# Kernel optimization log

Measured on AMD Instinct MI355X. Metric: run time of the kernel, lower is better.

## Reference

```python
import jax, jax.numpy as jnp
import numpy as np

EPS = 1e-5

def bn(x, g, b, mu, var):
    # inference-mode BatchNorm2d (InPlaceABNSync, activation='none')
    scale = g * jax.lax.rsqrt(var + EPS)
    shift = b - mu * scale
    return x * scale[None, :, None, None] + shift[None, :, None, None]

def conv1x1(x, w):
    # w: [C_out, C_in]; x: [B, C_in, H, W]
    return jnp.einsum('oc,bchw->bohw', w, x)

def block(x, w1, g1, b1, m1, v1, w2, g2, b2, m2, v2):
    # conv1x1 -> BN -> ReLU -> conv1x1 -> BN -> ReLU
    h = jax.nn.relu(bn(conv1x1(x, w1), g1, b1, m1, v1))
    return jax.nn.relu(bn(conv1x1(h, w2), g2, b2, m2, v2))

def setup_inputs() -> dict:
    key = jax.random.key(0)
    ks = jax.random.split(key, 24)
    B, HID, H, W = 8, 10, 512, 512
    MID = 32
    d = {}
    d['xf']  = jax.random.normal(ks[0], (B, HID, H, W), jnp.float32)
    d['xh1'] = jax.random.normal(ks[1], (B, HID, H, W), jnp.float32)
    d['xh2'] = jax.random.normal(ks[2], (B, HID, H, W), jnp.float32)
    def mk_bn(k, c):
        k1, k2, k3, k4 = jax.random.split(k, 4)
        return (jax.random.normal(k1, (c,), jnp.float32) * 0.1 + 1.0,
                jax.random.normal(k2, (c,), jnp.float32) * 0.1,
                jax.random.normal(k3, (c,), jnp.float32) * 0.1,
                jnp.abs(jax.random.normal(k4, (c,), jnp.float32)) * 0.5 + 0.5)
    # conv_hf params
    d['w_hf1'] = jax.random.normal(ks[3], (MID, 2 * HID), jnp.float32) * (1.0 / np.sqrt(2 * HID))
    d['g_hf1'], d['b_hf1'], d['m_hf1'], d['v_hf1'] = mk_bn(ks[4], MID)
    d['w_hf2'] = jax.random.normal(ks[5], (HID, MID), jnp.float32) * (1.0 / np.sqrt(MID))
    d['g_hf2'], d['b_hf2'], d['m_hf2'], d['v_hf2'] = mk_bn(ks[6], HID)
    # conv_update params
    d['w_up1'] = jax.random.normal(ks[7], (MID, 2 * HID), jnp.float32) * (1.0 / np.sqrt(2 * HID))
    d['g_up1'], d['b_up1'], d['m_up1'], d['v_up1'] = mk_bn(ks[8], MID)
    d['w_up2'] = jax.random.normal(ks[9], (HID, MID), jnp.float32) * (1.0 / np.sqrt(MID))
    d['g_up2'], d['b_up2'], d['m_up2'], d['v_up2'] = mk_bn(ks[10], HID)
    return d

def reference(xf, xh1, xh2,
              w_hf1, g_hf1, b_hf1, m_hf1, v_hf1,
              w_hf2, g_hf2, b_hf2, m_hf2, v_hf2,
              w_up1, g_up1, b_up1, m_up1, v_up1,
              w_up2, g_up2, b_up2, m_up2, v_up2):
    message = block(jnp.concatenate([xh1, xh2], axis=1),
                    w_hf1, g_hf1, b_hf1, m_hf1, v_hf1,
                    w_hf2, g_hf2, b_hf2, m_hf2, v_hf2)
    xf_new = block(jnp.concatenate([xf, message], axis=1),
                   w_up1, g_up1, b_up1, m_up1, v_up1,
                   w_up2, g_up2, b_up2, m_up2, v_up2)
    return (xf_new, message)
```

## Files before the change

### kernel.cpp

```cpp
#include <hip/hip_runtime.h>

#define EPS_BN 1e-5f
#define HW2 131072u
#define MSG_OFF 10485760u

typedef unsigned int u32;
typedef __fp16 h2 __attribute__((ext_vector_type(2)));

union W32 { u32 u; float f; h2 h; };

__device__ __forceinline__ float asf(u32 u){ W32 w; w.u = u; return w.f; }
__device__ __forceinline__ h2    ash(u32 u){ W32 w; w.u = u; return w.h; }
__device__ __forceinline__ u32 packh(float a, float b){
  W32 w; w.h.x = (__fp16)a; w.h.y = (__fp16)b; return w.u;
}

#if __has_builtin(__builtin_amdgcn_fdot2)
__device__ __forceinline__ float dot2(h2 a, h2 b, float c){
  return __builtin_amdgcn_fdot2(a, b, c, false);
}
#else
__device__ __forceinline__ float dot2(h2 a, h2 b, float c){
  return c + (float)a.x * (float)b.x + (float)a.y * (float)b.y;
}
#endif

#if __has_builtin(__builtin_amdgcn_cvt_pkrtz)
__device__ __forceinline__ h2 pk(float a, float b){ return __builtin_amdgcn_cvt_pkrtz(a, b); }
#else
__device__ __forceinline__ h2 pk(float a, float b){ h2 r; r.x = (__fp16)a; r.y = (__fp16)b; return r; }
#endif


extern "C" __global__ void prep_kernel(
  const float* __restrict__ w1, const float* __restrict__ g1, const float* __restrict__ b1, const float* __restrict__ m1, const float* __restrict__ v1,
  const float* __restrict__ w2, const float* __restrict__ g2, const float* __restrict__ b2, const float* __restrict__ m2, const float* __restrict__ v2,
  const float* __restrict__ w3, const float* __restrict__ g3, const float* __restrict__ b3, const float* __restrict__ m3, const float* __restrict__ v3,
  const float* __restrict__ w4, const float* __restrict__ g4, const float* __restrict__ b4, const float* __restrict__ m4, const float* __restrict__ v4,
  u32* __restrict__ ws)
{
  const int t = threadIdx.x;
  for (int i = t; i < 320; i += 256){ int cp = i >> 5, o = i & 31;
    float sc = g1[o] * rsqrtf(v1[o] + EPS_BN);
    ws[i] = packh(w1[o*20 + 2*cp] * sc, w1[o*20 + 2*cp + 1] * sc); }
  for (int i = t; i < 32; i += 256){
    float sc = g1[i] * rsqrtf(v1[i] + EPS_BN);
    W32 w; w.f = b1[i] - m1[i] * sc; ws[320 + i] = w.u; }
  for (int i = t; i < 256; i += 256){ int cp = i >> 4, o = i & 15; u32 val = 0u;
    if (o < 10){ float sc = g2[o] * rsqrtf(v2[o] + EPS_BN);
      val = packh(w2[o*32 + 2*cp] * sc, w2[o*32 + 2*cp + 1] * sc); }
    ws[352 + i] = val; }
  for (int i = t; i < 16; i += 256){ W32 w; w.f = 0.f;
    if (i < 10){ float sc = g2[i] * rsqrtf(v2[i] + EPS_BN); w.f = b2[i] - m2[i] * sc; }
    ws[608 + i] = w.u; }
  for (int i = t; i < 320; i += 256){ int cp = i >> 5, o = i & 31;
    float sc = g3[o] * rsqrtf(v3[o] + EPS_BN);
    ws[624 + i] = packh(w3[o*20 + 2*cp] * sc, w3[o*20 + 2*cp + 1] * sc); }
  for (int i = t; i < 32; i += 256){
    float sc = g3[i] * rsqrtf(v3[i] + EPS_BN);
    W32 w; w.f = b3[i] - m3[i] * sc; ws[944 + i] = w.u; }
  for (int i = t; i < 256; i += 256){ int cp = i >> 4, o = i & 15; u32 val = 0u;
    if (o < 10){ float sc = g4[o] * rsqrtf(v4[o] + EPS_BN);
      val = packh(w4[o*32 + 2*cp] * sc, w4[o*32 + 2*cp + 1] * sc); }
    ws[976 + i] = val; }
  for (int i = t; i < 16; i += 256){ W32 w; w.f = 0.f;
    if (i < 10){ float sc = g4[i] * rsqrtf(v4[i] + EPS_BN); w.f = b4[i] - m4[i] * sc; }
    ws[1232 + i] = w.u; }
}

#define DO4(AX, AY, HX, HY, Q, O0) \
  { h2 w0_ = ash((Q).x), w1_ = ash((Q).y), w2_ = ash((Q).z), w3_ = ash((Q).w); \
    AX[(O0)+0] = dot2(HX, w0_, AX[(O0)+0]); AY[(O0)+0] = dot2(HY, w0_, AY[(O0)+0]); \
    AX[(O0)+1] = dot2(HX, w1_, AX[(O0)+1]); AY[(O0)+1] = dot2(HY, w1_, AY[(O0)+1]); \
    AX[(O0)+2] = dot2(HX, w2_, AX[(O0)+2]); AY[(O0)+2] = dot2(HY, w2_, AY[(O0)+2]); \
    AX[(O0)+3] = dot2(HX, w3_, AX[(O0)+3]); AY[(O0)+3] = dot2(HY, w3_, AY[(O0)+3]); }

extern "C" __global__ __launch_bounds__(256) void fused_kernel(
  const float2* __restrict__ xf, const float2* __restrict__ xh1, const float2* __restrict__ xh2,
  const u32* __restrict__ wsp, float2* __restrict__ out)
{
  __shared__ __align__(16) u32 s[1248];
  for (int i = threadIdx.x; i < 1248; i += 256) s[i] = wsp[i];
  __syncthreads();

  const unsigned p  = blockIdx.x * 256u + threadIdx.x;
  const unsigned b  = p >> 17;
  const unsigned hw = p & (HW2 - 1u);
  const size_t base = (size_t)b * (10u * HW2) + hw;
  const float2* A1 = xh1 + base;
  const float2* A2 = xh2 + base;
  const float2* AF = xf  + base;

  float ax[32], ay[32];
  h2 px[10], py[10];

  #pragma unroll
  for (int o = 0; o < 32; o++){ float t = asf(s[320 + o]); ax[o] = t; ay[o] = t; }
  #pragma unroll
  for (int cp = 0; cp < 5; cp++){
    float2 c0 = A1[(size_t)(2*cp) * HW2];
    float2 c1 = A1[(size_t)(2*cp + 1) * HW2];
    px[cp] = pk(c0.x, c1.x); py[cp] = pk(c0.y, c1.y);
  }
  #pragma unroll
  for (int cp = 0; cp < 5; cp++){
    float2 c0 = A2[(size_t)(2*cp) * HW2];
    float2 c1 = A2[(size_t)(2*cp + 1) * HW2];
    px[5+cp] = pk(c0.x, c1.x); py[5+cp] = pk(c0.y, c1.y);
  }
  #pragma unroll
  for (int cp = 0; cp < 10; cp++){
    const uint4* wr = (const uint4*)&s[cp * 32];
    h2 hx = px[cp], hy = py[cp];
    #pragma unroll
    for (int j = 0; j < 8; j++){ uint4 q = wr[j]; DO4(ax, ay, hx, hy, q, 4*j); }
  }
  #pragma unroll
  for (int o = 0; o < 32; o++){ ax[o] = fmaxf(ax[o], 0.f); ay[o] = fmaxf(ay[o], 0.f); }

  float mx[10], my[10];
  #pragma unroll
  for (int o = 0; o < 10; o++){ float t = asf(s[608 + o]); mx[o] = t; my[o] = t; }
  h2 qx[16], qy[16];
  #pragma unroll
  for (int k = 0; k < 16; k++){ qx[k] = pk(ax[2*k], ax[2*k+1]); qy[k] = pk(ay[2*k], ay[2*k+1]); }
  #pragma unroll
  for (int cp = 0; cp < 16; cp++){
    const uint4* wr = (const uint4*)&s[352 + cp * 16];
    h2 hx = qx[cp], hy = qy[cp];
    uint4 q0 = wr[0]; DO4(mx, my, hx, hy, q0, 0);
    uint4 q1 = wr[1]; DO4(mx, my, hx, hy, q1, 4);
    uint4 q2 = wr[2];
    { h2 w0_ = ash(q2.x), w1_ = ash(q2.y);
      mx[8] = dot2(hx, w0_, mx[8]); my[8] = dot2(hy, w0_, my[8]);
      mx[9] = dot2(hx, w1_, mx[9]); my[9] = dot2(hy, w1_, my[9]); }
  }
  #pragma unroll
  for (int o = 0; o < 10; o++){ mx[o] = fmaxf(mx[o], 0.f); my[o] = fmaxf(my[o], 0.f); }
  #pragma unroll
  for (int o = 0; o < 10; o++){
    float2 r; r.x = mx[o]; r.y = my[o];
    out[MSG_OFF + base + (size_t)o * HW2] = r;
  }

  #pragma unroll
  for (int o = 0; o < 32; o++){ float t = asf(s[944 + o]); ax[o] = t; ay[o] = t; }
  #pragma unroll
  for (int cp = 0; cp < 5; cp++){
    float2 c0 = AF[(size_t)(2*cp) * HW2];
    float2 c1 = AF[(size_t)(2*cp + 1) * HW2];
    px[cp] = pk(c0.x, c1.x); py[cp] = pk(c0.y, c1.y);
  }
  #pragma unroll
  for (int k = 0; k < 5; k++){
    px[5+k] = pk(mx[2*k], mx[2*k+1]); py[5+k] = pk(my[2*k], my[2*k+1]);
  }
  #pragma unroll
  for (int cp = 0; cp < 10; cp++){
    const uint4* wr = (const uint4*)&s[624 + cp * 32];
    h2 hx = px[cp], hy = py[cp];
    #pragma unroll
    for (int j = 0; j < 8; j++){ uint4 q = wr[j]; DO4(ax, ay, hx, hy, q, 4*j); }
  }
  #pragma unroll
  for (int o = 0; o < 32; o++){ ax[o] = fmaxf(ax[o], 0.f); ay[o] = fmaxf(ay[o], 0.f); }

  float ox[10], oy[10];
  #pragma unroll
  for (int o = 0; o < 10; o++){ float t = asf(s[1232 + o]); ox[o] = t; oy[o] = t; }
  #pragma unroll
  for (int k = 0; k < 16; k++){ qx[k] = pk(ax[2*k], ax[2*k+1]); qy[k] = pk(ay[2*k], ay[2*k+1]); }
  #pragma unroll
  for (int cp = 0; cp < 16; cp++){
    const uint4* wr = (const uint4*)&s[976 + cp * 16];
    h2 hx = qx[cp], hy = qy[cp];
    uint4 q0 = wr[0]; DO4(ox, oy, hx, hy, q0, 0);
    uint4 q1 = wr[1]; DO4(ox, oy, hx, hy, q1, 4);
    uint4 q2 = wr[2];
    { h2 w0_ = ash(q2.x), w1_ = ash(q2.y);
      ox[8] = dot2(hx, w0_, ox[8]); oy[8] = dot2(hy, w0_, oy[8]);
      ox[9] = dot2(hx, w1_, ox[9]); oy[9] = dot2(hy, w1_, oy[9]); }
  }
  #pragma unroll
  for (int o = 0; o < 10; o++){
    float2 r; r.x = fmaxf(ox[o], 0.f); r.y = fmaxf(oy[o], 0.f);
    out[base + (size_t)o * HW2] = r;
  }
}

extern "C" void kernel_launch(void* const* d_in, const int* in_sizes, int n_in,
                              void* d_out, int out_size, void* d_ws, size_t ws_size,
                              hipStream_t stream)
{
  u32* ws = (u32*)d_ws;
  prep_kernel<<<1, 256, 0, stream>>>(
    (const float*)d_in[3],  (const float*)d_in[4],  (const float*)d_in[5],  (const float*)d_in[6],  (const float*)d_in[7],
    (const float*)d_in[8],  (const float*)d_in[9],  (const float*)d_in[10], (const float*)d_in[11], (const float*)d_in[12],
    (const float*)d_in[13], (const float*)d_in[14], (const float*)d_in[15], (const float*)d_in[16], (const float*)d_in[17],
    (const float*)d_in[18], (const float*)d_in[19], (const float*)d_in[20], (const float*)d_in[21], (const float*)d_in[22],
    ws);

  fused_kernel<<<4096, 256, 0, stream>>>(
    (const float2*)d_in[0], (const float2*)d_in[1], (const float2*)d_in[2],
    ws, (float2*)d_out);
}
```

Before: 381.5 us.

## Process four pixels per thread with float4 loads to amortize LDS weight reads

Each thread now handles four consecutive pixels instead of two, using float4 global loads and stores and halving the grid. Every weight fetched from shared memory is reused across four pixels, which cuts LDS traffic per FLOP, and bias initialization is folded into the first dot product. The xf load is moved earlier to overlap with compute, and launch bounds request two blocks per CU. The cost is much higher register pressure (a 32x4 accumulator array plus 16x4 packed halves), which may cause spills or lower occupancy on this memory-bound kernel.

```diff
diff --git a/kernel.cpp b/kernel.cpp
--- a/kernel.cpp
+++ b/kernel.cpp
@@ -1,8 +1,8 @@
 #include <hip/hip_runtime.h>
 
 #define EPS_BN 1e-5f
-#define HW2 131072u
-#define MSG_OFF 10485760u
+#define HW4 65536u
+#define MSG_OFF4 5242880u
 
 typedef unsigned int u32;
 typedef __fp16 h2 __attribute__((ext_vector_type(2)));
@@ -68,123 +68,166 @@
     ws[1232 + i] = w.u; }
 }
 
-#define DO4(AX, AY, HX, HY, Q, O0) \
+#define DO4x(A, H, Q, O0) \
   { h2 w0_ = ash((Q).x), w1_ = ash((Q).y), w2_ = ash((Q).z), w3_ = ash((Q).w); \
-    AX[(O0)+0] = dot2(HX, w0_, AX[(O0)+0]); AY[(O0)+0] = dot2(HY, w0_, AY[(O0)+0]); \
-    AX[(O0)+1] = dot2(HX, w1_, AX[(O0)+1]); AY[(O0)+1] = dot2(HY, w1_, AY[(O0)+1]); \
-    AX[(O0)+2] = dot2(HX, w2_, AX[(O0)+2]); AY[(O0)+2] = dot2(HY, w2_, AY[(O0)+2]); \
-    AX[(O0)+3] = dot2(HX, w3_, AX[(O0)+3]); AY[(O0)+3] = dot2(HY, w3_, AY[(O0)+3]); }
-
-extern "C" __global__ __launch_bounds__(256) void fused_kernel(
-  const float2* __restrict__ xf, const float2* __restrict__ xh1, const float2* __restrict__ xh2,
-  const u32* __restrict__ wsp, float2* __restrict__ out)
+    _Pragma("unroll") for (int j_ = 0; j_ < 4; j_++){ \
+      A[(O0)+0][j_] = dot2(H[j_], w0_, A[(O0)+0][j_]); \
+      A[(O0)+1][j_] = dot2(H[j_], w1_, A[(O0)+1][j_]); \
+      A[(O0)+2][j_] = dot2(H[j_], w2_, A[(O0)+2][j_]); \
+      A[(O0)+3][j_] = dot2(H[j_], w3_, A[(O0)+3][j_]); } }
+
+#define DO4i(A, H, Q, O0, BB) \
+  { h2 w0_ = ash((Q).x), w1_ = ash((Q).y), w2_ = ash((Q).z), w3_ = ash((Q).w); \
+    float b0_ = asf(s[(BB)+(O0)+0]), b1_ = asf(s[(BB)+(O0)+1]); \
+    float b2_ = asf(s[(BB)+(O0)+2]), b3_ = asf(s[(BB)+(O0)+3]); \
+    _Pragma("unroll") for (int j_ = 0; j_ < 4; j_++){ \
+      A[(O0)+0][j_] = dot2(H[j_], w0_, b0_); \
+      A[(O0)+1][j_] = dot2(H[j_], w1_, b1_); \
+      A[(O0)+2][j_] = dot2(H[j_], w2_, b2_); \
+      A[(O0)+3][j_] = dot2(H[j_], w3_, b3_); } }
+
+#define DO2x(A, H, Q2) \
+  { h2 w0_ = ash((Q2).x), w1_ = ash((Q2).y); \
+    _Pragma("unroll") for (int j_ = 0; j_ < 4; j_++){ \
+      A[8][j_] = dot2(H[j_], w0_, A[8][j_]); \
+      A[9][j_] = dot2(H[j_], w1_, A[9][j_]); } }
+
+#define DO2i(A, H, Q2, BB) \
+  { h2 w0_ = ash((Q2).x), w1_ = ash((Q2).y); \
+    float b8_ = asf(s[(BB)+8]), b9_ = asf(s[(BB)+9]); \
+    _Pragma("unroll") for (int j_ = 0; j_ < 4; j_++){ \
+      A[8][j_] = dot2(H[j_], w0_, b8_); \
+      A[9][j_] = dot2(H[j_], w1_, b9_); } }
+
+extern "C" __global__ __launch_bounds__(256, 2) void fused_kernel(
+  const float4* __restrict__ xf, const float4* __restrict__ xh1, const float4* __restrict__ xh2,
+  const u32* __restrict__ wsp, float4* __restrict__ out)
 {
   __shared__ __align__(16) u32 s[1248];
   for (int i = threadIdx.x; i < 1248; i += 256) s[i] = wsp[i];
   __syncthreads();
 
   const unsigned p  = blockIdx.x * 256u + threadIdx.x;
-  const unsigned b  = p >> 17;
-  const unsigned hw = p & (HW2 - 1u);
-  const size_t base = (size_t)b * (10u * HW2) + hw;
-  const float2* A1 = xh1 + base;
-  const float2* A2 = xh2 + base;
-  const float2* AF = xf  + base;
-
-  float ax[32], ay[32];
-  h2 px[10], py[10];
-
-  #pragma unroll
-  for (int o = 0; o < 32; o++){ float t = asf(s[320 + o]); ax[o] = t; ay[o] = t; }
+  const unsigned b  = p >> 16;
+  const unsigned hw = p & (HW4 - 1u);
+  const size_t base = (size_t)b * (10u * HW4) + hw;
+  const float4* A1 = xh1 + base;
+  const float4* A2 = xh2 + base;
+  const float4* AF = xf  + base;
+
+  float a[32][4];
+  h2 ph[10][4];
+
   #pragma unroll
   for (int cp = 0; cp < 5; cp++){
-    float2 c0 = A1[(size_t)(2*cp) * HW2];
-    float2 c1 = A1[(size_t)(2*cp + 1) * HW2];
-    px[cp] = pk(c0.x, c1.x); py[cp] = pk(c0.y, c1.y);
+    float4 c0 = A1[(size_t)(2*cp)     * HW4];
+    float4 c1 = A1[(size_t)(2*cp + 1) * HW4];
+    ph[cp][0] = pk(c0.x, c1.x); ph[cp][1] = pk(c0.y, c1.y);
+    ph[cp][2] = pk(c0.z, c1.z); ph[cp][3] = pk(c0.w, c1.w);
   }
   #pragma unroll
   for (int cp = 0; cp < 5; cp++){
-    float2 c0 = A2[(size_t)(2*cp) * HW2];
-    float2 c1 = A2[(size_t)(2*cp + 1) * HW2];
-    px[5+cp] = pk(c0.x, c1.x); py[5+cp] = pk(c0.y, c1.y);
-  }
-  #pragma unroll
-  for (int cp = 0; cp < 10; cp++){
+    float4 c0 = A2[(size_t)(2*cp)     * HW4];
+    float4 c1 = A2[(size_t)(2*cp + 1) * HW4];
+    ph[5+cp][0] = pk(c0.x, c1.x); ph[5+cp][1] = pk(c0.y, c1.y);
+    ph[5+cp][2] = pk(c0.z, c1.z); ph[5+cp][3] = pk(c0.w, c1.w);
+  }
+
+  { const uint4* wr = (const uint4*)&s[0];
+    #pragma unroll
+    for (int jw = 0; jw < 8; jw++){ uint4 q = wr[jw]; DO4i(a, ph[0], q, 4*jw, 320); } }
+  #pragma unroll
+  for (int cp = 1; cp < 10; cp++){
     const uint4* wr = (const uint4*)&s[cp * 32];
-    h2 hx = px[cp], hy = py[cp];
-    #pragma unroll
-    for (int j = 0; j < 8; j++){ uint4 q = wr[j]; DO4(ax, ay, hx, hy, q, 4*j); }
-  }
-  #pragma unroll
-  for (int o = 0; o < 32; o++){ ax[o] = fmaxf(ax[o], 0.f); ay[o] = fmaxf(ay[o], 0.f); }
-
-  float mx[10], my[10];
-  #pragma unroll
-  for (int o = 0; o < 10; o++){ float t = asf(s[608 + o]); mx[o] = t; my[o] = t; }
-  h2 qx[16], qy[16];
-  #pragma unroll
-  for (int k = 0; k < 16; k++){ qx[k] = pk(ax[2*k], ax[2*k+1]); qy[k] = pk(ay[2*k], ay[2*k+1]); }
-  #pragma unroll
-  for (int cp = 0; cp < 16; cp++){
+    #pragma unroll
+    for (int jw = 0; jw < 8; jw++){ uint4 q = wr[jw]; DO4x(a, ph[cp], q, 4*jw); }
+  }
+  #pragma unroll
+  for (int o = 0; o < 32; o++){
+    #pragma unroll
+    for (int j = 0; j < 4; j++) a[o][j] = fmaxf(a[o][j], 0.f);
+  }
+
+  #pragma unroll
+  for (int cp = 0; cp < 5; cp++){
+    float4 c0 = AF[(size_t)(2*cp)     * HW4];
+    float4 c1 = AF[(size_t)(2*cp + 1) * HW4];
+    ph[cp][0] = pk(c0.x, c1.x); ph[cp][1] = pk(c0.y, c1.y);
+    ph[cp][2] = pk(c0.z, c1.z); ph[cp][3] = pk(c0.w, c1.w);
+  }
+
+  h2 qh[16][4];
+  #pragma unroll
+  for (int k = 0; k < 16; k++){
+    #pragma unroll
+    for (int j = 0; j < 4; j++) qh[k][j] = pk(a[2*k][j], a[2*k+1][j]);
+  }
+  float m[10][4];
+  { const uint4* wr = (const uint4*)&s[352];
+    uint4 q0 = wr[0]; DO4i(m, qh[0], q0, 0, 608);
+    uint4 q1 = wr[1]; DO4i(m, qh[0], q1, 4, 608);
+    uint4 q2 = wr[2]; DO2i(m, qh[0], q2, 608); }
+  #pragma unroll
+  for (int cp = 1; cp < 16; cp++){
     const uint4* wr = (const uint4*)&s[352 + cp * 16];
-    h2 hx = qx[cp], hy = qy[cp];
-    uint4 q0 = wr[0]; DO4(mx, my, hx, hy, q0, 0);
-    uint4 q1 = wr[1]; DO4(mx, my, hx, hy, q1, 4);
-    uint4 q2 = wr[2];
-    { h2 w0_ = ash(q2.x), w1_ = ash(q2.y);
-      mx[8] = dot2(hx, w0_, mx[8]); my[8] = dot2(hy, w0_, my[8]);
-      mx[9] = dot2(hx, w1_, mx[9]); my[9] = dot2(hy, w1_, my[9]); }
-  }
-  #pragma unroll
-  for (int o = 0; o < 10; o++){ mx[o] = fmaxf(mx[o], 0.f); my[o] = fmaxf(my[o], 0.f); }
+    uint4 q0 = wr[0]; DO4x(m, qh[cp], q0, 0);
+    uint4 q1 = wr[1]; DO4x(m, qh[cp], q1, 4);
+    uint4 q2 = wr[2]; DO2x(m, qh[cp], q2);
+  }
   #pragma unroll
   for (int o = 0; o < 10; o++){
-    float2 r; r.x = mx[o]; r.y = my[o];
-    out[MSG_OFF + base + (size_t)o * HW2] = r;
-  }
-
-  #pragma unroll
-  for (int o = 0; o < 32; o++){ float t = asf(s[944 + o]); ax[o] = t; ay[o] = t; }
-  #pragma unroll
-  for (int cp = 0; cp < 5; cp++){
-    float2 c0 = AF[(size_t)(2*cp) * HW2];
-    float2 c1 = AF[(size_t)(2*cp + 1) * HW2];
-    px[cp] = pk(c0.x, c1.x); py[cp] = pk(c0.y, c1.y);
-  }
+    #pragma unroll
+    for (int j = 0; j < 4; j++) m[o][j] = fmaxf(m[o][j], 0.f);
+  }
+  #pragma unroll
+  for (int o = 0; o < 10; o++){
+    float4 r; r.x = m[o][0]; r.y = m[o][1]; r.z = m[o][2]; r.w = m[o][3];
+    out[MSG_OFF4 + base + (size_t)o * HW4] = r;
+  }
+
   #pragma unroll
   for (int k = 0; k < 5; k++){
-    px[5+k] = pk(mx[2*k], mx[2*k+1]); py[5+k] = pk(my[2*k], my[2*k+1]);
-  }
-  #pragma unroll
-  for (int cp = 0; cp < 10; cp++){
+    #pragma unroll
+    for (int j = 0; j < 4; j++) ph[5+k][j] = pk(m[2*k][j], m[2*k+1][j]);
+  }
+  { const uint4* wr = (const uint4*)&s[624];
+    #pragma unroll
+    for (int jw = 0; jw < 8; jw++){ uint4 q = wr[jw]; DO4i(a, ph[0], q, 4*jw, 944); } }
+  #pragma unroll
+  for (int cp = 1; cp < 10; cp++){
     const uint4* wr = (const uint4*)&s[624 + cp * 32];
-    h2 hx = px[cp], hy = py[cp];
-    #pragma unroll
-    for (int j = 0; j < 8; j++){ uint4 q = wr[j]; DO4(ax, ay, hx, hy, q, 4*j); }
-  }
-  #pragma unroll
-  for (int o = 0; o < 32; o++){ ax[o] = fmaxf(ax[o], 0.f); ay[o] = fmaxf(ay[o], 0.f); }
-
-  float ox[10], oy[10];
-  #pragma unroll
-  for (int o = 0; o < 10; o++){ float t = asf(s[1232 + o]); ox[o] = t; oy[o] = t; }
-  #pragma unroll
-  for (int k = 0; k < 16; k++){ qx[k] = pk(ax[2*k], ax[2*k+1]); qy[k] = pk(ay[2*k], ay[2*k+1]); }
-  #pragma unroll
-  for (int cp = 0; cp < 16; cp++){
+    #pragma unroll
+    for (int jw = 0; jw < 8; jw++){ uint4 q = wr[jw]; DO4x(a, ph[cp], q, 4*jw); }
+  }
+  #pragma unroll
+  for (int o = 0; o < 32; o++){
+    #pragma unroll
+    for (int j = 0; j < 4; j++) a[o][j] = fmaxf(a[o][j], 0.f);
+  }
+
+  #pragma unroll
+  for (int k = 0; k < 16; k++){
+    #pragma unroll
+    for (int j = 0; j < 4; j++) qh[k][j] = pk(a[2*k][j], a[2*k+1][j]);
+  }
+  float oo[10][4];
+  { const uint4* wr = (const uint4*)&s[976];
+    uint4 q0 = wr[0]; DO4i(oo, qh[0], q0, 0, 1232);
+    uint4 q1 = wr[1]; DO4i(oo, qh[0], q1, 4, 1232);
+    uint4 q2 = wr[2]; DO2i(oo, qh[0], q2, 1232); }
+  #pragma unroll
+  for (int cp = 1; cp < 16; cp++){
     const uint4* wr = (const uint4*)&s[976 + cp * 16];
-    h2 hx = qx[cp], hy = qy[cp];
-    uint4 q0 = wr[0]; DO4(ox, oy, hx, hy, q0, 0);
-    uint4 q1 = wr[1]; DO4(ox, oy, hx, hy, q1, 4);
-    uint4 q2 = wr[2];
-    { h2 w0_ = ash(q2.x), w1_ = ash(q2.y);
-      ox[8] = dot2(hx, w0_, ox[8]); oy[8] = dot2(hy, w0_, oy[8]);
-      ox[9] = dot2(hx, w1_, ox[9]); oy[9] = dot2(hy, w1_, oy[9]); }
+    uint4 q0 = wr[0]; DO4x(oo, qh[cp], q0, 0);
+    uint4 q1 = wr[1]; DO4x(oo, qh[cp], q1, 4);
+    uint4 q2 = wr[2]; DO2x(oo, qh[cp], q2);
   }
   #pragma unroll
   for (int o = 0; o < 10; o++){
-    float2 r; r.x = fmaxf(ox[o], 0.f); r.y = fmaxf(oy[o], 0.f);
-    out[base + (size_t)o * HW2] = r;
+    float4 r;
+    r.x = fmaxf(oo[o][0], 0.f); r.y = fmaxf(oo[o][1], 0.f);
+    r.z = fmaxf(oo[o][2], 0.f); r.w = fmaxf(oo[o][3], 0.f);
+    out[base + (size_t)o * HW4] = r;
   }
 }
 
@@ -200,7 +243,7 @@
     (const float*)d_in[18], (const float*)d_in[19], (const float*)d_in[20], (const float*)d_in[21], (const float*)d_in[22],
     ws);
 
-  fused_kernel<<<4096, 256, 0, stream>>>(
-    (const float2*)d_in[0], (const float2*)d_in[1], (const float2*)d_in[2],
-    ws, (float2*)d_out);
-}
+  fused_kernel<<<2048, 256, 0, stream>>>(
+    (const float4*)d_in[0], (const float4*)d_in[1], (const float4*)d_in[2],
+    ws, (float4*)d_out);
+}
```

Result: slower. 390.0 us (+2.2%).

## Read folded weights directly from global memory, fold bias into first dot, hoist xf loads

Applied to the files above, without the earlier changes.

Removes the shared-memory staging of the 1248-word weight table and its block barrier. Weights are now read straight from the global workspace; they are uniform across the wavefront, so the compiler may turn them into scalar loads. Bias initialisation is folded into the first dot2 of each layer instead of a separate copy loop. The xf input loads are moved earlier, ahead of the message layer, to overlap their latency with compute. The cost is many more global/scalar loads per thread and higher register pressure from the earlier xf loads.

```diff
diff --git a/kernel.cpp b/kernel.cpp
--- a/kernel.cpp
+++ b/kernel.cpp
@@ -75,13 +75,20 @@
     AX[(O0)+2] = dot2(HX, w2_, AX[(O0)+2]); AY[(O0)+2] = dot2(HY, w2_, AY[(O0)+2]); \
     AX[(O0)+3] = dot2(HX, w3_, AX[(O0)+3]); AY[(O0)+3] = dot2(HY, w3_, AY[(O0)+3]); }
 
+#define DO4i(AX, AY, HX, HY, Q, O0, BB) \
+  { h2 w0_ = ash((Q).x), w1_ = ash((Q).y), w2_ = ash((Q).z), w3_ = ash((Q).w); \
+    float b0_ = asf(s[(BB)+(O0)+0]), b1_ = asf(s[(BB)+(O0)+1]); \
+    float b2_ = asf(s[(BB)+(O0)+2]), b3_ = asf(s[(BB)+(O0)+3]); \
+    AX[(O0)+0] = dot2(HX, w0_, b0_); AY[(O0)+0] = dot2(HY, w0_, b0_); \
+    AX[(O0)+1] = dot2(HX, w1_, b1_); AY[(O0)+1] = dot2(HY, w1_, b1_); \
+    AX[(O0)+2] = dot2(HX, w2_, b2_); AY[(O0)+2] = dot2(HY, w2_, b2_); \
+    AX[(O0)+3] = dot2(HX, w3_, b3_); AY[(O0)+3] = dot2(HY, w3_, b3_); }
+
 extern "C" __global__ __launch_bounds__(256) void fused_kernel(
   const float2* __restrict__ xf, const float2* __restrict__ xh1, const float2* __restrict__ xh2,
   const u32* __restrict__ wsp, float2* __restrict__ out)
 {
-  __shared__ __align__(16) u32 s[1248];
-  for (int i = threadIdx.x; i < 1248; i += 256) s[i] = wsp[i];
-  __syncthreads();
+  const u32* __restrict__ s = wsp;
 
   const unsigned p  = blockIdx.x * 256u + threadIdx.x;
   const unsigned b  = p >> 17;
@@ -95,8 +102,6 @@
   h2 px[10], py[10];
 
   #pragma unroll
-  for (int o = 0; o < 32; o++){ float t = asf(s[320 + o]); ax[o] = t; ay[o] = t; }
-  #pragma unroll
   for (int cp = 0; cp < 5; cp++){
     float2 c0 = A1[(size_t)(2*cp) * HW2];
     float2 c1 = A1[(size_t)(2*cp + 1) * HW2];
@@ -108,8 +113,13 @@
     float2 c1 = A2[(size_t)(2*cp + 1) * HW2];
     px[5+cp] = pk(c0.x, c1.x); py[5+cp] = pk(c0.y, c1.y);
   }
-  #pragma unroll
-  for (int cp = 0; cp < 10; cp++){
+
+  { const uint4* wr = (const uint4*)&s[0];
+    h2 hx = px[0], hy = py[0];
+    #pragma unroll
+    for (int j = 0; j < 8; j++){ uint4 q = wr[j]; DO4i(ax, ay, hx, hy, q, 4*j, 320); } }
+  #pragma unroll
+  for (int cp = 1; cp < 10; cp++){
     const uint4* wr = (const uint4*)&s[cp * 32];
     h2 hx = px[cp], hy = py[cp];
     #pragma unroll
@@ -118,14 +128,28 @@
   #pragma unroll
   for (int o = 0; o < 32; o++){ ax[o] = fmaxf(ax[o], 0.f); ay[o] = fmaxf(ay[o], 0.f); }
 
+  #pragma unroll
+  for (int cp = 0; cp < 5; cp++){
+    float2 c0 = AF[(size_t)(2*cp) * HW2];
+    float2 c1 = AF[(size_t)(2*cp + 1) * HW2];
+    px[cp] = pk(c0.x, c1.x); py[cp] = pk(c0.y, c1.y);
+  }
+
   float mx[10], my[10];
-  #pragma unroll
-  for (int o = 0; o < 10; o++){ float t = asf(s[608 + o]); mx[o] = t; my[o] = t; }
   h2 qx[16], qy[16];
   #pragma unroll
   for (int k = 0; k < 16; k++){ qx[k] = pk(ax[2*k], ax[2*k+1]); qy[k] = pk(ay[2*k], ay[2*k+1]); }
-  #pragma unroll
-  for (int cp = 0; cp < 16; cp++){
+  { const uint4* wr = (const uint4*)&s[352];
+    h2 hx = qx[0], hy = qy[0];
+    uint4 q0 = wr[0]; DO4i(mx, my, hx, hy, q0, 0, 608);
+    uint4 q1 = wr[1]; DO4i(mx, my, hx, hy, q1, 4, 608);
+    uint4 q2 = wr[2];
+    { h2 w0_ = ash(q2.x), w1_ = ash(q2.y);
+      float b8_ = asf(s[608+8]), b9_ = asf(s[608+9]);
+      mx[8] = dot2(hx, w0_, b8_); my[8] = dot2(hy, w0_, b8_);
+      mx[9] = dot2(hx, w1_, b9_); my[9] = dot2(hy, w1_, b9_); } }
+  #pragma unroll
+  for (int cp = 1; cp < 16; cp++){
     const uint4* wr = (const uint4*)&s[352 + cp * 16];
     h2 hx = qx[cp], hy = qy[cp];
     uint4 q0 = wr[0]; DO4(mx, my, hx, hy, q0, 0);
@@ -144,19 +168,15 @@
   }
 
   #pragma unroll
-  for (int o = 0; o < 32; o++){ float t = asf(s[944 + o]); ax[o] = t; ay[o] = t; }
-  #pragma unroll
-  for (int cp = 0; cp < 5; cp++){
-    float2 c0 = AF[(size_t)(2*cp) * HW2];
-    float2 c1 = AF[(size_t)(2*cp + 1) * HW2];
-    px[cp] = pk(c0.x, c1.x); py[cp] = pk(c0.y, c1.y);
-  }
-  #pragma unroll
   for (int k = 0; k < 5; k++){
     px[5+k] = pk(mx[2*k], mx[2*k+1]); py[5+k] = pk(my[2*k], my[2*k+1]);
   }
-  #pragma unroll
-  for (int cp = 0; cp < 10; cp++){
+  { const uint4* wr = (const uint4*)&s[624];
+    h2 hx = px[0], hy = py[0];
+    #pragma unroll
+    for (int j = 0; j < 8; j++){ uint4 q = wr[j]; DO4i(ax, ay, hx, hy, q, 4*j, 944); } }
+  #pragma unroll
+  for (int cp = 1; cp < 10; cp++){
     const uint4* wr = (const uint4*)&s[624 + cp * 32];
     h2 hx = px[cp], hy = py[cp];
     #pragma unroll
@@ -167,11 +187,18 @@
 
   float ox[10], oy[10];
   #pragma unroll
-  for (int o = 0; o < 10; o++){ float t = asf(s[1232 + o]); ox[o] = t; oy[o] = t; }
-  #pragma unroll
   for (int k = 0; k < 16; k++){ qx[k] = pk(ax[2*k], ax[2*k+1]); qy[k] = pk(ay[2*k], ay[2*k+1]); }
-  #pragma unroll
-  for (int cp = 0; cp < 16; cp++){
+  { const uint4* wr = (const uint4*)&s[976];
+    h2 hx = qx[0], hy = qy[0];
+    uint4 q0 = wr[0]; DO4i(ox, oy, hx, hy, q0, 0, 1232);
+    uint4 q1 = wr[1]; DO4i(ox, oy, hx, hy, q1, 4, 1232);
+    uint4 q2 = wr[2];
+    { h2 w0_ = ash(q2.x), w1_ = ash(q2.y);
+      float b8_ = asf(s[1232+8]), b9_ = asf(s[1232+9]);
+      ox[8] = dot2(hx, w0_, b8_); oy[8] = dot2(hy, w0_, b8_);
+      ox[9] = dot2(hx, w1_, b9_); oy[9] = dot2(hy, w1_, b9_); } }
+  #pragma unroll
+  for (int cp = 1; cp < 16; cp++){
     const uint4* wr = (const uint4*)&s[976 + cp * 16];
     h2 hx = qx[cp], hy = qy[cp];
     uint4 q0 = wr[0]; DO4(ox, oy, hx, hy, q0, 0);
```

New measurement: 393.1 us. 1.03x slower.

## Compute fused 1x1 conv blocks with MFMA 16x16x32 f16 instead of dot2

Applied to the files above, without the earlier changes.

Replaces the per-thread fdot2 accumulation of all four 1x1 convolutions with MFMA 16x16x32 f16 instructions. Each wave now processes 16-pixel tiles in a loop, and the prep kernel packs weights into MFMA operand layouts with permuted K ordering. Weights live in registers rather than shared memory. The aim is to remove the ALU bottleneck, in exchange for narrower 64-byte coalesced global accesses and a complex lane/channel mapping.

```diff
diff --git a/kernel.cpp b/kernel.cpp
--- a/kernel.cpp
+++ b/kernel.cpp
@@ -1,36 +1,34 @@
 #include <hip/hip_runtime.h>
 
 #define EPS_BN 1e-5f
-#define HW2 131072u
-#define MSG_OFF 10485760u
+#define PLANE  262144u
+#define IMG10  2621440u
+#define MSGF   20971520u
 
 typedef unsigned int u32;
 typedef __fp16 h2 __attribute__((ext_vector_type(2)));
+typedef _Float16 v8h __attribute__((ext_vector_type(8)));
+typedef float v4f __attribute__((ext_vector_type(4)));
 
 union W32 { u32 u; float f; h2 h; };
-
-__device__ __forceinline__ float asf(u32 u){ W32 w; w.u = u; return w.f; }
-__device__ __forceinline__ h2    ash(u32 u){ W32 w; w.u = u; return w.h; }
+union AB  { u32 u[4]; uint4 q; v8h h; };
+
 __device__ __forceinline__ u32 packh(float a, float b){
   W32 w; w.h.x = (__fp16)a; w.h.y = (__fp16)b; return w.u;
 }
 
-#if __has_builtin(__builtin_amdgcn_fdot2)
-__device__ __forceinline__ float dot2(h2 a, h2 b, float c){
-  return __builtin_amdgcn_fdot2(a, b, c, false);
+#if __has_builtin(__builtin_amdgcn_cvt_pkrtz)
+__device__ __forceinline__ u32 pku(float a, float b){
+  W32 w; w.h = __builtin_amdgcn_cvt_pkrtz(a, b); return w.u;
 }
 #else
-__device__ __forceinline__ float dot2(h2 a, h2 b, float c){
-  return c + (float)a.x * (float)b.x + (float)a.y * (float)b.y;
-}
+__device__ __forceinline__ u32 pku(float a, float b){ return packh(a, b); }
 #endif
 
-#if __has_builtin(__builtin_amdgcn_cvt_pkrtz)
-__device__ __forceinline__ h2 pk(float a, float b){ return __builtin_amdgcn_cvt_pkrtz(a, b); }
-#else
-__device__ __forceinline__ h2 pk(float a, float b){ h2 r; r.x = (__fp16)a; r.y = (__fp16)b; return r; }
-#endif
-
+
+__device__ __forceinline__ float wv(const float* w, int ncol, int row, int k){
+  return (k >= 0) ? w[row*ncol + k] : 0.f;
+}
 
 extern "C" __global__ void prep_kernel(
   const float* __restrict__ w1, const float* __restrict__ g1, const float* __restrict__ b1, const float* __restrict__ m1, const float* __restrict__ v1,
@@ -40,151 +38,170 @@
   u32* __restrict__ ws)
 {
   const int t = threadIdx.x;
-  for (int i = t; i < 320; i += 256){ int cp = i >> 5, o = i & 31;
-    float sc = g1[o] * rsqrtf(v1[o] + EPS_BN);
-    ws[i] = packh(w1[o*20 + 2*cp] * sc, w1[o*20 + 2*cp + 1] * sc); }
+
+  for (int r = 0; r < 2; r++){
+    for (int i = t; i < 256; i += 256){
+      int lane = i >> 2, tq = i & 3, g = lane >> 4, m = (lane & 15) + 16*r;
+      int ka, kb;
+      if      (tq == 0){ ka = g;                      kb = 4 + g; }
+      else if (tq == 1){ ka = (g < 2) ? 8 + g : -1;   kb = 10 + g; }
+      else if (tq == 2){ ka = 14 + g;                 kb = (g < 2) ? 18 + g : -1; }
+      else             { ka = -1;                     kb = -1; }
+      float sc = g1[m] * rsqrtf(v1[m] + EPS_BN);
+      ws[256*r + i] = packh(wv(w1, 20, m, ka) * sc, wv(w1, 20, m, kb) * sc);
+    }
+  }
+  for (int i = t; i < 256; i += 256){
+    int lane = i >> 2, tq = i & 3, g = lane >> 4, m = lane & 15;
+    int k0 = (tq < 2) ? (4*g + 2*tq) : (16 + 4*g + 2*(tq - 2));
+    u32 val = 0u;
+    if (m < 10){
+      float sc = g2[m] * rsqrtf(v2[m] + EPS_BN);
+      val = packh(w2[m*32 + k0] * sc, w2[m*32 + k0 + 1] * sc);
+    }
+    ws[512 + i] = val;
+  }
+  for (int r = 0; r < 2; r++){
+    for (int i = t; i < 256; i += 256){
+      int lane = i >> 2, tq = i & 3, g = lane >> 4, m = (lane & 15) + 16*r;
+      int ka = -1, kb = -1;
+      if (g == 0){ const int base[4] = {10, 12, 0, 2}; ka = base[tq]; kb = ka + 1; }
+      else if (g == 1){ const int base[4] = {14, 16, 4, 6}; ka = base[tq]; kb = ka + 1; }
+      else if (g == 2){ if (tq == 0){ ka = 18; kb = 19; } else if (tq == 1){ ka = 8; kb = 9; } }
+      float sc = g3[m] * rsqrtf(v3[m] + EPS_BN);
+      ws[768 + 256*r + i] = packh(wv(w3, 20, m, ka) * sc, wv(w3, 20, m, kb) * sc);
+    }
+  }
+  for (int i = t; i < 256; i += 256){
+    int lane = i >> 2, tq = i & 3, g = lane >> 4, m = lane & 15;
+    int k0 = (tq < 2) ? (4*g + 2*tq) : (16 + 4*g + 2*(tq - 2));
+    u32 val = 0u;
+    if (m < 10){
+      float sc = g4[m] * rsqrtf(v4[m] + EPS_BN);
+      val = packh(w4[m*32 + k0] * sc, w4[m*32 + k0 + 1] * sc);
+    }
+    ws[1280 + i] = val;
+  }
   for (int i = t; i < 32; i += 256){
     float sc = g1[i] * rsqrtf(v1[i] + EPS_BN);
-    W32 w; w.f = b1[i] - m1[i] * sc; ws[320 + i] = w.u; }
-  for (int i = t; i < 256; i += 256){ int cp = i >> 4, o = i & 15; u32 val = 0u;
-    if (o < 10){ float sc = g2[o] * rsqrtf(v2[o] + EPS_BN);
-      val = packh(w2[o*32 + 2*cp] * sc, w2[o*32 + 2*cp + 1] * sc); }
-    ws[352 + i] = val; }
-  for (int i = t; i < 16; i += 256){ W32 w; w.f = 0.f;
+    W32 w; w.f = b1[i] - m1[i] * sc; ws[1536 + i] = w.u;
+  }
+  for (int i = t; i < 16; i += 256){
+    W32 w; w.f = 0.f;
     if (i < 10){ float sc = g2[i] * rsqrtf(v2[i] + EPS_BN); w.f = b2[i] - m2[i] * sc; }
-    ws[608 + i] = w.u; }
-  for (int i = t; i < 320; i += 256){ int cp = i >> 5, o = i & 31;
-    float sc = g3[o] * rsqrtf(v3[o] + EPS_BN);
-    ws[624 + i] = packh(w3[o*20 + 2*cp] * sc, w3[o*20 + 2*cp + 1] * sc); }
+    ws[1568 + i] = w.u;
+  }
   for (int i = t; i < 32; i += 256){
     float sc = g3[i] * rsqrtf(v3[i] + EPS_BN);
-    W32 w; w.f = b3[i] - m3[i] * sc; ws[944 + i] = w.u; }
-  for (int i = t; i < 256; i += 256){ int cp = i >> 4, o = i & 15; u32 val = 0u;
-    if (o < 10){ float sc = g4[o] * rsqrtf(v4[o] + EPS_BN);
-      val = packh(w4[o*32 + 2*cp] * sc, w4[o*32 + 2*cp + 1] * sc); }
-    ws[976 + i] = val; }
-  for (int i = t; i < 16; i += 256){ W32 w; w.f = 0.f;
+    W32 w; w.f = b3[i] - m3[i] * sc; ws[1584 + i] = w.u;
+  }
+  for (int i = t; i < 16; i += 256){
+    W32 w; w.f = 0.f;
     if (i < 10){ float sc = g4[i] * rsqrtf(v4[i] + EPS_BN); w.f = b4[i] - m4[i] * sc; }
-    ws[1232 + i] = w.u; }
-}
-
-#define DO4(AX, AY, HX, HY, Q, O0) \
-  { h2 w0_ = ash((Q).x), w1_ = ash((Q).y), w2_ = ash((Q).z), w3_ = ash((Q).w); \
-    AX[(O0)+0] = dot2(HX, w0_, AX[(O0)+0]); AY[(O0)+0] = dot2(HY, w0_, AY[(O0)+0]); \
-    AX[(O0)+1] = dot2(HX, w1_, AX[(O0)+1]); AY[(O0)+1] = dot2(HY, w1_, AY[(O0)+1]); \
-    AX[(O0)+2] = dot2(HX, w2_, AX[(O0)+2]); AY[(O0)+2] = dot2(HY, w2_, AY[(O0)+2]); \
-    AX[(O0)+3] = dot2(HX, w3_, AX[(O0)+3]); AY[(O0)+3] = dot2(HY, w3_, AY[(O0)+3]); }
+    ws[1616 + i] = w.u;
+  }
+}
+
+__device__ __forceinline__ v4f mfma16(const AB& a, const AB& b, v4f c){
+  return __builtin_amdgcn_mfma_f32_16x16x32_f16(a.h, b.h, c, 0, 0, 0);
+}
 
 extern "C" __global__ __launch_bounds__(256) void fused_kernel(
-  const float2* __restrict__ xf, const float2* __restrict__ xh1, const float2* __restrict__ xh2,
-  const u32* __restrict__ wsp, float2* __restrict__ out)
+  const float* __restrict__ xf, const float* __restrict__ xh1, const float* __restrict__ xh2,
+  const u32* __restrict__ wsp, float* __restrict__ out)
 {
-  __shared__ __align__(16) u32 s[1248];
-  for (int i = threadIdx.x; i < 1248; i += 256) s[i] = wsp[i];
-  __syncthreads();
-
-  const unsigned p  = blockIdx.x * 256u + threadIdx.x;
-  const unsigned b  = p >> 17;
-  const unsigned hw = p & (HW2 - 1u);
-  const size_t base = (size_t)b * (10u * HW2) + hw;
-  const float2* A1 = xh1 + base;
-  const float2* A2 = xh2 + base;
-  const float2* AF = xf  + base;
-
-  float ax[32], ay[32];
-  h2 px[10], py[10];
-
-  #pragma unroll
-  for (int o = 0; o < 32; o++){ float t = asf(s[320 + o]); ax[o] = t; ay[o] = t; }
-  #pragma unroll
-  for (int cp = 0; cp < 5; cp++){
-    float2 c0 = A1[(size_t)(2*cp) * HW2];
-    float2 c1 = A1[(size_t)(2*cp + 1) * HW2];
-    px[cp] = pk(c0.x, c1.x); py[cp] = pk(c0.y, c1.y);
-  }
-  #pragma unroll
-  for (int cp = 0; cp < 5; cp++){
-    float2 c0 = A2[(size_t)(2*cp) * HW2];
-    float2 c1 = A2[(size_t)(2*cp + 1) * HW2];
-    px[5+cp] = pk(c0.x, c1.x); py[5+cp] = pk(c0.y, c1.y);
-  }
-  #pragma unroll
-  for (int cp = 0; cp < 10; cp++){
-    const uint4* wr = (const uint4*)&s[cp * 32];
-    h2 hx = px[cp], hy = py[cp];
-    #pragma unroll
-    for (int j = 0; j < 8; j++){ uint4 q = wr[j]; DO4(ax, ay, hx, hy, q, 4*j); }
-  }
-  #pragma unroll
-  for (int o = 0; o < 32; o++){ ax[o] = fmaxf(ax[o], 0.f); ay[o] = fmaxf(ay[o], 0.f); }
-
-  float mx[10], my[10];
-  #pragma unroll
-  for (int o = 0; o < 10; o++){ float t = asf(s[608 + o]); mx[o] = t; my[o] = t; }
-  h2 qx[16], qy[16];
-  #pragma unroll
-  for (int k = 0; k < 16; k++){ qx[k] = pk(ax[2*k], ax[2*k+1]); qy[k] = pk(ay[2*k], ay[2*k+1]); }
-  #pragma unroll
-  for (int cp = 0; cp < 16; cp++){
-    const uint4* wr = (const uint4*)&s[352 + cp * 16];
-    h2 hx = qx[cp], hy = qy[cp];
-    uint4 q0 = wr[0]; DO4(mx, my, hx, hy, q0, 0);
-    uint4 q1 = wr[1]; DO4(mx, my, hx, hy, q1, 4);
-    uint4 q2 = wr[2];
-    { h2 w0_ = ash(q2.x), w1_ = ash(q2.y);
-      mx[8] = dot2(hx, w0_, mx[8]); my[8] = dot2(hy, w0_, my[8]);
-      mx[9] = dot2(hx, w1_, mx[9]); my[9] = dot2(hy, w1_, my[9]); }
-  }
-  #pragma unroll
-  for (int o = 0; o < 10; o++){ mx[o] = fmaxf(mx[o], 0.f); my[o] = fmaxf(my[o], 0.f); }
-  #pragma unroll
-  for (int o = 0; o < 10; o++){
-    float2 r; r.x = mx[o]; r.y = my[o];
-    out[MSG_OFF + base + (size_t)o * HW2] = r;
-  }
-
-  #pragma unroll
-  for (int o = 0; o < 32; o++){ float t = asf(s[944 + o]); ax[o] = t; ay[o] = t; }
-  #pragma unroll
-  for (int cp = 0; cp < 5; cp++){
-    float2 c0 = AF[(size_t)(2*cp) * HW2];
-    float2 c1 = AF[(size_t)(2*cp + 1) * HW2];
-    px[cp] = pk(c0.x, c1.x); py[cp] = pk(c0.y, c1.y);
-  }
-  #pragma unroll
-  for (int k = 0; k < 5; k++){
-    px[5+k] = pk(mx[2*k], mx[2*k+1]); py[5+k] = pk(my[2*k], my[2*k+1]);
-  }
-  #pragma unroll
-  for (int cp = 0; cp < 10; cp++){
-    const uint4* wr = (const uint4*)&s[624 + cp * 32];
-    h2 hx = px[cp], hy = py[cp];
-    #pragma unroll
-    for (int j = 0; j < 8; j++){ uint4 q = wr[j]; DO4(ax, ay, hx, hy, q, 4*j); }
-  }
-  #pragma unroll
-  for (int o = 0; o < 32; o++){ ax[o] = fmaxf(ax[o], 0.f); ay[o] = fmaxf(ay[o], 0.f); }
-
-  float ox[10], oy[10];
-  #pragma unroll
-  for (int o = 0; o < 10; o++){ float t = asf(s[1232 + o]); ox[o] = t; oy[o] = t; }
-  #pragma unroll
-  for (int k = 0; k < 16; k++){ qx[k] = pk(ax[2*k], ax[2*k+1]); qy[k] = pk(ay[2*k], ay[2*k+1]); }
-  #pragma unroll
-  for (int cp = 0; cp < 16; cp++){
-    const uint4* wr = (const uint4*)&s[976 + cp * 16];
-    h2 hx = qx[cp], hy = qy[cp];
-    uint4 q0 = wr[0]; DO4(ox, oy, hx, hy, q0, 0);
-    uint4 q1 = wr[1]; DO4(ox, oy, hx, hy, q1, 4);
-    uint4 q2 = wr[2];
-    { h2 w0_ = ash(q2.x), w1_ = ash(q2.y);
-      ox[8] = dot2(hx, w0_, ox[8]); oy[8] = dot2(hy, w0_, oy[8]);
-      ox[9] = dot2(hx, w1_, ox[9]); oy[9] = dot2(hy, w1_, oy[9]); }
-  }
-  #pragma unroll
-  for (int o = 0; o < 10; o++){
-    float2 r; r.x = fmaxf(ox[o], 0.f); r.y = fmaxf(oy[o], 0.f);
-    out[base + (size_t)o * HW2] = r;
+  const unsigned tid  = threadIdx.x;
+  const unsigned lane = tid & 63u;
+  const unsigned c    = lane & 15u;
+  const unsigned g    = lane >> 4;
+
+  const uint4* W = (const uint4*)wsp;
+  AB f1a, f1b, f2w, f3a, f3b, f4w;
+  f1a.q = W[lane];        f1b.q = W[64 + lane];
+  f2w.q = W[128 + lane];
+  f3a.q = W[192 + lane];  f3b.q = W[256 + lane];
+  f4w.q = W[320 + lane];
+  const v4f* Bv = (const v4f*)(wsp + 1536);
+  v4f c1a = Bv[g];
+  v4f c1b = Bv[4 + g];
+  v4f c2  = Bv[8 + g];
+  v4f c3a = Bv[12 + g];
+  v4f c3b = Bv[16 + g];
+  v4f c4  = Bv[20 + g];
+
+  const u32 soff0 = g * PLANE + c;
+  const u32 soff1 = (4 + g) * PLANE + c;
+  const u32 soff2 = (8 + g) * PLANE + c;
+  const u32 xoff0 = (4*g + 0) * PLANE + c;
+  const u32 xoff1 = (4*g + 1) * PLANE + c;
+  const u32 xoff2 = (4*g + 2) * PLANE + c;
+  const u32 xoff3 = (4*g + 3) * PLANE + c;
+  const bool v8  = (g < 2);
+  const bool vj0 = (4*g + 0 < 10), vj1 = (4*g + 1 < 10);
+  const bool vj2 = (4*g + 2 < 10), vj3 = (4*g + 3 < 10);
+
+  const unsigned wgl = blockIdx.x * 4u + (tid >> 6);
+
+  #pragma unroll 2
+  for (int it = 0; it < 16; ++it){
+    const unsigned tile = wgl * 16u + it;
+    const unsigned gp   = tile << 4;
+    const unsigned b    = gp >> 18;
+    const unsigned hw   = gp & (PLANE - 1u);
+    const u32 pt = b * IMG10 + hw;
+
+    float L0 = xh1[pt + soff0];
+    float L1 = xh1[pt + soff1];
+    float L2 = v8 ? xh1[pt + soff2] : 0.f;
+    float L3 = xh2[pt + soff0];
+    float L4 = xh2[pt + soff1];
+    float L5 = v8 ? xh2[pt + soff2] : 0.f;
+    float X0 = vj0 ? xf[pt + xoff0] : 0.f;
+    float X1 = vj1 ? xf[pt + xoff1] : 0.f;
+    float X2 = vj2 ? xf[pt + xoff2] : 0.f;
+    float X3 = vj3 ? xf[pt + xoff3] : 0.f;
+
+    AB b1u;
+    b1u.u[0] = pku(L0, L1); b1u.u[1] = pku(L2, L3);
+    b1u.u[2] = pku(L4, L5); b1u.u[3] = 0u;
+    v4f d0 = mfma16(f1a, b1u, c1a);
+    v4f d1 = mfma16(f1b, b1u, c1b);
+    d0.x = fmaxf(d0.x, 0.f); d0.y = fmaxf(d0.y, 0.f); d0.z = fmaxf(d0.z, 0.f); d0.w = fmaxf(d0.w, 0.f);
+    d1.x = fmaxf(d1.x, 0.f); d1.y = fmaxf(d1.y, 0.f); d1.z = fmaxf(d1.z, 0.f); d1.w = fmaxf(d1.w, 0.f);
+
+    AB hb;
+    hb.u[0] = pku(d0.x, d0.y); hb.u[1] = pku(d0.z, d0.w);
+    hb.u[2] = pku(d1.x, d1.y); hb.u[3] = pku(d1.z, d1.w);
+    v4f dm = mfma16(f2w, hb, c2);
+    dm.x = fmaxf(dm.x, 0.f); dm.y = fmaxf(dm.y, 0.f); dm.z = fmaxf(dm.z, 0.f); dm.w = fmaxf(dm.w, 0.f);
+
+    if (vj0) out[MSGF + pt + xoff0] = dm.x;
+    if (vj1) out[MSGF + pt + xoff1] = dm.y;
+    if (vj2) out[MSGF + pt + xoff2] = dm.z;
+    if (vj3) out[MSGF + pt + xoff3] = dm.w;
+
+    u32 mt0 = pku(dm.x, dm.y), mt1 = pku(dm.z, dm.w);
+    u32 xt0 = pku(X0, X1),     xt1 = pku(X2, X3);
+    AB b3u;
+    b3u.u[0] = mt0;
+    b3u.u[1] = (g == 2) ? xt0 : mt1;
+    b3u.u[2] = xt0;
+    b3u.u[3] = xt1;
+    v4f e0 = mfma16(f3a, b3u, c3a);
+    v4f e1 = mfma16(f3b, b3u, c3b);
+    e0.x = fmaxf(e0.x, 0.f); e0.y = fmaxf(e0.y, 0.f); e0.z = fmaxf(e0.z, 0.f); e0.w = fmaxf(e0.w, 0.f);
+    e1.x = fmaxf(e1.x, 0.f); e1.y = fmaxf(e1.y, 0.f); e1.z = fmaxf(e1.z, 0.f); e1.w = fmaxf(e1.w, 0.f);
+
+    AB hb2;
+    hb2.u[0] = pku(e0.x, e0.y); hb2.u[1] = pku(e0.z, e0.w);
+    hb2.u[2] = pku(e1.x, e1.y); hb2.u[3] = pku(e1.z, e1.w);
+    v4f dq = mfma16(f4w, hb2, c4);
+    dq.x = fmaxf(dq.x, 0.f); dq.y = fmaxf(dq.y, 0.f); dq.z = fmaxf(dq.z, 0.f); dq.w = fmaxf(dq.w, 0.f);
+
+    if (vj0) out[pt + xoff0] = dq.x;
+    if (vj1) out[pt + xoff1] = dq.y;
+    if (vj2) out[pt + xoff2] = dq.z;
+    if (vj3) out[pt + xoff3] = dq.w;
   }
 }
 
@@ -200,7 +217,7 @@
     (const float*)d_in[18], (const float*)d_in[19], (const float*)d_in[20], (const float*)d_in[21], (const float*)d_in[22],
     ws);
 
-  fused_kernel<<<4096, 256, 0, stream>>>(
-    (const float2*)d_in[0], (const float2*)d_in[1], (const float2*)d_in[2],
-    ws, (float2*)d_out);
-}
+  fused_kernel<<<2048, 256, 0, stream>>>(
+    (const float*)d_in[0], (const float*)d_in[1], (const float*)d_in[2],
+    ws, (float*)d_out);
+}
```

Result: slower. 426.8 us (+11.9%).
